# Kernel tuning notes

Hardware: AMD Instinct MI355X
Metric: run time of the kernel (lower is better)

Reference implementation:

```python
import jax, jax.numpy as jnp
import numpy as np

N_HEAD = 12


def setup_inputs() -> dict:
    key = jax.random.key(0)
    ks = jax.random.split(key, 5)
    B, T, C = 2, 2048, 768
    x = jax.random.normal(ks[0], (B, T, C), dtype=jnp.float32)
    w_attn = jax.random.normal(ks[1], (3 * C, C), dtype=jnp.float32) * 0.02
    b_attn = jax.random.normal(ks[2], (3 * C,), dtype=jnp.float32) * 0.02
    w_proj = jax.random.normal(ks[3], (C, C), dtype=jnp.float32) * 0.02
    b_proj = jax.random.normal(ks[4], (C,), dtype=jnp.float32) * 0.02
    return {"x": x, "w_attn": w_attn, "b_attn": b_attn, "w_proj": w_proj, "b_proj": b_proj}


def reference(x, w_attn, b_attn, w_proj, b_proj):
    B, T, C = x.shape
    H = N_HEAD
    D = C // H
    # fused QKV projection (torch Linear: x @ W.T + b)
    qkv = x @ w_attn.T + b_attn                      # [B, T, 3C]
    q, k, v = jnp.split(qkv, 3, axis=-1)
    q = q.reshape(B, T, H, D).transpose(0, 2, 1, 3)  # [B, H, T, D]
    k = k.reshape(B, T, H, D).transpose(0, 2, 1, 3)
    v = v.reshape(B, T, H, D).transpose(0, 2, 1, 3)
    # NOTE: original scales by 1/sqrt(k.size(0)) == 1/sqrt(B) (batch!), reproduced faithfully
    scale = 1.0 / jnp.sqrt(jnp.asarray(B, dtype=x.dtype))
    scores = jnp.einsum("bhtd,bhsd->bhts", q, k) * scale  # [B, H, T, T]
    causal = jnp.tril(jnp.ones((T, T), dtype=bool))
    scores = jnp.where(causal[None, None], scores, jnp.asarray(-jnp.inf, dtype=x.dtype))
    attn = jax.nn.softmax(scores, axis=-1)
    # dropout layers are identity in eval mode
    out = jnp.einsum("bhts,bhsd->bhtd", attn, v)     # [B, H, T, D]
    out = out.transpose(0, 2, 1, 3).reshape(B, T, C)
    return out @ w_proj.T + b_proj
```

## Files before the change

kernel.cpp:

```cpp
#include <hip/hip_runtime.h>
#include <hip/hip_bf16.h>
#include <stdint.h>

typedef __bf16 bf16;
typedef __bf16 bf16x4 __attribute__((ext_vector_type(4)));
typedef __bf16 bf16x8 __attribute__((ext_vector_type(8)));
typedef float f32x4 __attribute__((ext_vector_type(4)));

__device__ __forceinline__ f32x4 mfma16(bf16x8 a, bf16x8 b, f32x4 c) {
    return __builtin_amdgcn_mfma_f32_16x16x32_bf16(a, b, c, 0, 0, 0);
}

__device__ __forceinline__ void gload_lds16(const void* g, void* l) {
    __builtin_amdgcn_global_load_lds((__attribute__((address_space(1))) void*)g,
                                     (__attribute__((address_space(3))) void*)l,
                                     16, 0, 0);
}

__global__ void k_cast3(const float* __restrict__ x, const float* __restrict__ wa,
                        const float* __restrict__ wp, bf16* __restrict__ xb,
                        bf16* __restrict__ wab, bf16* __restrict__ wpb) {
    const int N1 = 786432, N2 = 442368, N3 = 147456;
    int i = blockIdx.x * blockDim.x + threadIdx.x;
    int stride = gridDim.x * blockDim.x;
    for (; i < N1 + N2 + N3; i += stride) {
        const float* src; bf16* dst; int j = i;
        if (j < N1)           { src = x;  dst = xb; }
        else if (j < N1 + N2) { src = wa; dst = wab; j -= N1; }
        else                  { src = wp; dst = wpb; j -= N1 + N2; }
        float4 v = reinterpret_cast<const float4*>(src)[j];
        bf16x4 o = { (bf16)v.x, (bf16)v.y, (bf16)v.z, (bf16)v.w };
        reinterpret_cast<bf16x4*>(dst)[j] = o;
    }
}

template<bool BF16_OUT>
__global__ __launch_bounds__(256) void k_gemm_bt(
        const bf16* __restrict__ A, const bf16* __restrict__ W,
        const float* __restrict__ bias, void* __restrict__ Cout,
        int M, int N, int K) {
    __shared__ bf16 As[128 * 64];
    __shared__ bf16 Ws[128 * 64];
    const int tid = threadIdx.x;
    const int l = tid & 63, w = tid >> 6;
    const int lr = l & 15, lq = l >> 4;
    const int wm = w >> 1, wn = w & 1;
    const int bm = blockIdx.y * 128, bn = blockIdx.x * 128;

    f32x4 acc[4][4] = {};

    for (int k0 = 0; k0 < K; k0 += 64) {
        __syncthreads();
        #pragma unroll
        for (int i = 0; i < 4; ++i) {
            int c = tid + i * 256;
            int row = c >> 3, j = c & 7;
            int src8 = (j ^ (row & 7)) * 8;
            gload_lds16(A + (size_t)(bm + row) * K + k0 + src8, As + c * 8);
            gload_lds16(W + (size_t)(bn + row) * K + k0 + src8, Ws + c * 8);
        }
        __syncthreads();
        bf16x8 af[2][4], wf[2][4];
        #pragma unroll
        for (int ks = 0; ks < 2; ++ks)
            #pragma unroll
            for (int f = 0; f < 4; ++f) {
                int ra = wm * 64 + f * 16 + lr;
                int rb = wn * 64 + f * 16 + lr;
                af[ks][f] = *reinterpret_cast<const bf16x8*>(
                    As + ra * 64 + (((ks * 4 + lq) ^ (lr & 7)) * 8));
                wf[ks][f] = *reinterpret_cast<const bf16x8*>(
                    Ws + rb * 64 + (((ks * 4 + lq) ^ (lr & 7)) * 8));
            }
        #pragma unroll
        for (int ks = 0; ks < 2; ++ks)
            #pragma unroll
            for (int fm = 0; fm < 4; ++fm)
                #pragma unroll
                for (int fn = 0; fn < 4; ++fn)
                    acc[fm][fn] = mfma16(af[ks][fm], wf[ks][fn], acc[fm][fn]);
    }

    #pragma unroll
    for (int fm = 0; fm < 4; ++fm) {
        #pragma unroll
        for (int fn = 0; fn < 4; ++fn) {
            int row = bm + wm * 64 + fm * 16 + lq * 4;
            int col = bn + wn * 64 + fn * 16 + lr;
            float bv = bias[col];
            #pragma unroll
            for (int r = 0; r < 4; ++r) {
                float v = acc[fm][fn][r] + bv;
                if (BF16_OUT)
                    ((bf16*)Cout)[(size_t)(row + r) * N + col] = (bf16)v;
                else
                    ((float*)Cout)[(size_t)(row + r) * N + col] = v;
            }
        }
    }
}

__global__ __launch_bounds__(256) void k_transV(const bf16* __restrict__ qkv,
                                                bf16* __restrict__ vT) {
    const int g = blockIdx.x;
    const int bh = g >> 4, tc = g & 15;
    const int h = bh % 12, b = bh / 12;
    const int t0 = tc * 128;
    __shared__ bf16 Lt[128][68];
    const bf16* src = qkv + (size_t)(b * 2048 + t0) * 2304 + 1536 + h * 64;
    const int tid = threadIdx.x;
    #pragma unroll
    for (int ii = 0; ii < 4; ++ii) {
        int tt = ii * 32 + (tid >> 3);
        int ch = tid & 7;
        bf16x8 v = *reinterpret_cast<const bf16x8*>(src + (size_t)tt * 2304 + ch * 8);
        union { bf16x8 v8; bf16x4 h4[2]; } u; u.v8 = v;
        *reinterpret_cast<bf16x4*>(&Lt[tt][ch * 8])     = u.h4[0];
        *reinterpret_cast<bf16x4*>(&Lt[tt][ch * 8 + 4]) = u.h4[1];
    }
    __syncthreads();
    bf16* dst = vT + (size_t)bh * 64 * 2048 + t0;
    const int d = tid >> 2;
    #pragma unroll
    for (int ii = 0; ii < 4; ++ii) {
        int tch = ii * 4 + (tid & 3);
        bf16x8 v;
        #pragma unroll
        for (int e = 0; e < 8; ++e) v[e] = Lt[tch * 8 + e][d];
        *reinterpret_cast<bf16x8*>(&dst[(size_t)d * 2048 + tch * 8]) = v;
    }
}

#define CLOG2E 1.02014439f

__global__ __launch_bounds__(256, 3) void k_flash_attn(
        const bf16* __restrict__ qkv, const bf16* __restrict__ vT,
        bf16* __restrict__ att, float* __restrict__ part, int mode) {
    __shared__ bf16 Ks[3][4096];
    __shared__ bf16 VTs[3][4096];

    const int tid = threadIdx.x;
    const int l = tid & 63, w = tid >> 6;
    const int lr = l & 15, lq = l >> 4;

    const int bid = blockIdx.x;
    int qb, h, b, jt0, jt1, slot;
    bool dopart;
    if (mode) {
        int bh = bid % 24, idx = bid / 24;
        h = bh % 12; b = bh / 12;
        if (idx < 16)      { qb = 16 + idx;  jt0 = 0;  jt1 = 16;     dopart = true;  slot = (bh * 16 + idx) * 2; }
        else if (idx < 32) { qb = 47 - idx;  jt0 = 16; jt1 = qb + 1; dopart = true;  slot = (bh * 16 + (qb - 16)) * 2 + 1; }
        else               { qb = 47 - idx;  jt0 = 0;  jt1 = qb + 1; dopart = false; slot = 0; }
    } else {
        const int s = bid >> 8, i = (bid >> 3) & 31, t7 = bid & 7;
        if (s == 0)      qb = i;
        else if (s == 2) qb = (i + 16) & 31;
        else             qb = (i < 8) ? (31 - 2 * i) : (i < 16) ? (30 - 2 * i)
                           : (i < 24) ? (62 - 2 * i) : (63 - 2 * i);
        const int hb = s * 8 + t7;
        h = hb % 12; b = hb / 12;
        jt0 = 0; jt1 = qb + 1; dopart = false; slot = 0;
    }

    const bf16* Qp  = qkv + (size_t)b * 2048 * 2304 + h * 64;
    const bf16* Kp  = Qp + 768;
    const bf16* Vtp = vT + (size_t)(b * 12 + h) * 64 * 2048;

    const int qr0 = qb * 64 + w * 16;

    bf16x8 qf[2];
    #pragma unroll
    for (int ks = 0; ks < 2; ++ks)
        qf[ks] = *reinterpret_cast<const bf16x8*>(
            Qp + (size_t)(qr0 + lr) * 2304 + ks * 32 + lq * 8);

    f32x4 o[4] = {};
    float lsum = 0.f;

    auto stageK = [&](int buf, int kv0) {
        #pragma unroll
        for (int ii = 0; ii < 2; ++ii) {
            int c = tid + ii * 256;
            int row = c >> 3, j = c & 7;
            gload_lds16(Kp + (size_t)(kv0 + row) * 2304 + ((j ^ (row & 7)) * 8),
                        &Ks[buf][c * 8]);
        }
    };
    auto stageV = [&](int buf, int kv0) {
        #pragma unroll
        for (int ii = 0; ii < 2; ++ii) {
            int c = tid + ii * 256;
            int row = c >> 3, j = c & 7;
            gload_lds16(Vtp + (size_t)row * 2048 + kv0 + ((j ^ (row & 7)) * 8),
                        &VTs[buf][c * 8]);
        }
    };

    stageK(0, jt0 * 64);
    stageV(0, jt0 * 64);
    const bool two = (jt1 > jt0 + 1);
    if (two) { stageK(1, jt0 * 64 + 64); stageV(1, jt0 * 64 + 64); }
    if (two) asm volatile("s_waitcnt vmcnt(4)" ::: "memory");
    else     asm volatile("s_waitcnt vmcnt(0)" ::: "memory");
    __builtin_amdgcn_s_barrier();
    asm volatile("" ::: "memory");

    for (int jt = jt0; jt < jt1; ++jt) {
        const int cur = (jt - jt0) % 3;
        const int kv0 = jt * 64;
        if (jt + 2 < jt1) {
            stageK((jt + 2 - jt0) % 3, kv0 + 128);
            stageV((jt + 2 - jt0) % 3, kv0 + 128);
        }

        const bool diag = (jt == qb);
        const int rsw = lr & 7;
        float p[4][4];
        __builtin_amdgcn_s_setprio(1);
        #pragma unroll
        for (int t = 0; t < 4; ++t) {
            f32x4 sacc = {0.f, 0.f, 0.f, 0.f};
            #pragma unroll
            for (int ks = 0; ks < 2; ++ks) {
                bf16x8 kf = *reinterpret_cast<const bf16x8*>(
                    &Ks[cur][(t * 16 + lr) * 64 + (((ks * 4 + lq) ^ rsw) * 8)]);
                sacc = mfma16(kf, qf[ks], sacc);
            }
            #pragma unroll
            for (int r = 0; r < 4; ++r)
                p[t][r] = __builtin_amdgcn_exp2f(sacc[r] * CLOG2E);
        }
        __builtin_amdgcn_s_setprio(0);
        if (diag) {
            #pragma unroll
            for (int t = 0; t < 4; ++t)
                #pragma unroll
                for (int r = 0; r < 4; ++r)
                    if (t * 16 + lq * 4 + r > w * 16 + lr) p[t][r] = 0.f;
        }
        {
            float s0 = (p[0][0] + p[0][1]) + (p[0][2] + p[0][3]);
            float s1 = (p[1][0] + p[1][1]) + (p[1][2] + p[1][3]);
            float s2 = (p[2][0] + p[2][1]) + (p[2][2] + p[2][3]);
            float s3 = (p[3][0] + p[3][1]) + (p[3][2] + p[3][3]);
            lsum += (s0 + s1) + (s2 + s3);
        }

        unsigned P0[4], P1[4];
        #pragma unroll
        for (int t = 0; t < 4; ++t) {
            asm("v_cvt_pk_bf16_f32 %0, %1, %2" : "=v"(P0[t]) : "v"(p[t][0]), "v"(p[t][1]));
            asm("v_cvt_pk_bf16_f32 %0, %1, %2" : "=v"(P1[t]) : "v"(p[t][2]), "v"(p[t][3]));
        }
        #pragma unroll
        for (int ks = 0; ks < 2; ++ks) {
            unsigned a0 = P0[2 * ks], b0 = P0[2 * ks + 1];
            asm volatile("v_permlane32_swap_b32 %0, %1" : "+v"(a0), "+v"(b0));
            asm volatile("v_permlane16_swap_b32 %0, %1" : "+v"(a0), "+v"(b0));
            unsigned a1 = P1[2 * ks], b1 = P1[2 * ks + 1];
            asm volatile("v_permlane32_swap_b32 %0, %1" : "+v"(a1), "+v"(b1));
            asm volatile("v_permlane16_swap_b32 %0, %1" : "+v"(a1), "+v"(b1));
            union { unsigned u[4]; bf16x8 v8; } pk_;
            pk_.u[0] = a0; pk_.u[1] = a1; pk_.u[2] = b0; pk_.u[3] = b1;
            bf16x8 pa = pk_.v8;
            __builtin_amdgcn_s_setprio(1);
            #pragma unroll
            for (int db = 0; db < 4; ++db) {
                bf16x8 vf = *reinterpret_cast<const bf16x8*>(
                    &VTs[cur][(db * 16 + lr) * 64 + (((ks * 4 + lq) ^ rsw) * 8)]);
                o[db] = mfma16(pa, vf, o[db]);
            }
            __builtin_amdgcn_s_setprio(0);
        }

        if (jt + 1 < jt1) {
            if (jt + 2 < jt1) asm volatile("s_waitcnt vmcnt(4)" ::: "memory");
            else              asm volatile("s_waitcnt vmcnt(0)" ::: "memory");
        }
        __builtin_amdgcn_s_barrier();
        asm volatile("" ::: "memory");
    }

    lsum += __shfl_xor(lsum, 16);
    lsum += __shfl_xor(lsum, 32);

    if (dopart) {
        float* pb = part + (size_t)slot * 4160;
        #pragma unroll
        for (int db = 0; db < 4; ++db)
            #pragma unroll
            for (int r = 0; r < 4; ++r)
                pb[(w * 16 + lq * 4 + r) * 64 + db * 16 + lr] = o[db][r];
        if (lq == 0) pb[4096 + w * 16 + lr] = lsum;
    } else {
        float inv[4];
        #pragma unroll
        for (int r = 0; r < 4; ++r)
            inv[r] = 1.0f / __shfl(lsum, lq * 4 + r);
        #pragma unroll
        for (int db = 0; db < 4; ++db)
            #pragma unroll
            for (int r = 0; r < 4; ++r) {
                float v = o[db][r] * inv[r];
                att[(size_t)(b * 2048 + qr0 + lq * 4 + r) * 768 + h * 64 + db * 16 + lr] = (bf16)v;
            }
    }
}

__global__ __launch_bounds__(256) void k_attn_reduce(
        const float* __restrict__ part, bf16* __restrict__ att) {
    int g = blockIdx.x;
    int bh = g / 16, q16 = g % 16, qb = 16 + q16;
    int h = bh % 12, b = bh / 12;
    const float* p0 = part + (size_t)((bh * 16 + q16) * 2) * 4160;
    const float* p1 = p0 + 4160;
    for (int e = threadIdx.x; e < 4096; e += 256) {
        int row = e >> 6, col = e & 63;
        float O = p0[e] + p1[e];
        float L = p0[4096 + row] + p1[4096 + row];
        att[(size_t)(b * 2048 + qb * 64 + row) * 768 + h * 64 + col] = (bf16)(O / L);
    }
}

extern "C" void kernel_launch(void* const* d_in, const int* in_sizes, int n_in,
                              void* d_out, int out_size, void* d_ws, size_t ws_size,
                              hipStream_t stream) {
    const float* x      = (const float*)d_in[0];
    const float* w_attn = (const float*)d_in[1];
    const float* b_attn = (const float*)d_in[2];
    const float* w_proj = (const float*)d_in[3];
    const float* b_proj = (const float*)d_in[4];

    char* ws = (char*)d_ws;
    bf16* xb   = (bf16*)(ws + 0);
    bf16* vT   = (bf16*)(ws + 0);
    bf16* wab  = (bf16*)(ws + 6291456);
    bf16* wpb  = (bf16*)(ws + 9830400);
    bf16* qkv  = (bf16*)(ws + 11010048);
    bf16* att  = (bf16*)(ws + 29884416);
    float* part = (float*)(ws + 36175872);
    const unsigned long long WS_NEEDED = 36175872ull + 12779520ull;

    k_cast3<<<2048, 256, 0, stream>>>(x, w_attn, w_proj, xb, wab, wpb);

    dim3 g1(2304 / 128, 4096 / 128);
    k_gemm_bt<true><<<g1, 256, 0, stream>>>(xb, wab, b_attn, qkv, 4096, 2304, 768);

    k_transV<<<384, 256, 0, stream>>>(qkv, vT);

    if (ws_size >= WS_NEEDED) {
        k_flash_attn<<<1152, 256, 0, stream>>>(qkv, vT, att, part, 1);
        k_attn_reduce<<<384, 256, 0, stream>>>(part, att);
    } else {
        k_flash_attn<<<768, 256, 0, stream>>>(qkv, vT, att, part, 0);
    }

    dim3 g2(768 / 128, 4096 / 128);
    k_gemm_bt<false><<<g2, 256, 0, stream>>>(att, wpb, b_proj, d_out, 4096, 768, 768);
}
```

Measured before the change: 91.53 us.

## Process two query tiles per attention block and narrow output-projection GEMM tile

Each flash-attention block now handles 128 query rows (two 64-row tiles) and reuses every staged K/V tile for both, halving K/V global loads and LDS staging per query row. The causal skip for the upper tile is handled with a per-iteration active flag, and the split-K partial/reduce layout is rebuilt for 128-row blocks with a new work assignment. Separately, the output-projection GEMM is templated to a 64-wide N tile, doubling its grid so more CUs are busy. The cost is more registers for doubled accumulators, fewer attention blocks in flight, and some wasted masking work on diagonal tiles.

```diff
diff --git a/kernel.cpp b/kernel.cpp
--- a/kernel.cpp
+++ b/kernel.cpp
@@ -34,20 +34,21 @@
     }
 }
 
-template<bool BF16_OUT>
+template<int BN, bool BF16_OUT>
 __global__ __launch_bounds__(256) void k_gemm_bt(
         const bf16* __restrict__ A, const bf16* __restrict__ W,
         const float* __restrict__ bias, void* __restrict__ Cout,
         int M, int N, int K) {
+    constexpr int FN = BN / 32;
     __shared__ bf16 As[128 * 64];
-    __shared__ bf16 Ws[128 * 64];
+    __shared__ bf16 Ws[BN * 64];
     const int tid = threadIdx.x;
     const int l = tid & 63, w = tid >> 6;
     const int lr = l & 15, lq = l >> 4;
     const int wm = w >> 1, wn = w & 1;
-    const int bm = blockIdx.y * 128, bn = blockIdx.x * 128;
-
-    f32x4 acc[4][4] = {};
+    const int bm = blockIdx.y * 128, bn = blockIdx.x * BN;
+
+    f32x4 acc[4][FN] = {};
 
     for (int k0 = 0; k0 < K; k0 += 64) {
         __syncthreads();
@@ -57,36 +58,46 @@
             int row = c >> 3, j = c & 7;
             int src8 = (j ^ (row & 7)) * 8;
             gload_lds16(A + (size_t)(bm + row) * K + k0 + src8, As + c * 8);
+        }
+        #pragma unroll
+        for (int i = 0; i < FN; ++i) {
+            int c = tid + i * 256;
+            int row = c >> 3, j = c & 7;
+            int src8 = (j ^ (row & 7)) * 8;
             gload_lds16(W + (size_t)(bn + row) * K + k0 + src8, Ws + c * 8);
         }
         __syncthreads();
-        bf16x8 af[2][4], wf[2][4];
-        #pragma unroll
-        for (int ks = 0; ks < 2; ++ks)
+        bf16x8 af[2][4], wf[2][FN];
+        #pragma unroll
+        for (int ks = 0; ks < 2; ++ks) {
             #pragma unroll
             for (int f = 0; f < 4; ++f) {
                 int ra = wm * 64 + f * 16 + lr;
-                int rb = wn * 64 + f * 16 + lr;
                 af[ks][f] = *reinterpret_cast<const bf16x8*>(
                     As + ra * 64 + (((ks * 4 + lq) ^ (lr & 7)) * 8));
+            }
+            #pragma unroll
+            for (int f = 0; f < FN; ++f) {
+                int rb = wn * (FN * 16) + f * 16 + lr;
                 wf[ks][f] = *reinterpret_cast<const bf16x8*>(
                     Ws + rb * 64 + (((ks * 4 + lq) ^ (lr & 7)) * 8));
             }
+        }
         #pragma unroll
         for (int ks = 0; ks < 2; ++ks)
             #pragma unroll
             for (int fm = 0; fm < 4; ++fm)
                 #pragma unroll
-                for (int fn = 0; fn < 4; ++fn)
+                for (int fn = 0; fn < FN; ++fn)
                     acc[fm][fn] = mfma16(af[ks][fm], wf[ks][fn], acc[fm][fn]);
     }
 
     #pragma unroll
     for (int fm = 0; fm < 4; ++fm) {
         #pragma unroll
-        for (int fn = 0; fn < 4; ++fn) {
+        for (int fn = 0; fn < FN; ++fn) {
             int row = bm + wm * 64 + fm * 16 + lq * 4;
-            int col = bn + wn * 64 + fn * 16 + lr;
+            int col = bn + wn * (FN * 16) + fn * 16 + lr;
             float bv = bias[col];
             #pragma unroll
             for (int r = 0; r < 4; ++r) {
@@ -147,36 +158,41 @@
     int qb, h, b, jt0, jt1, slot;
     bool dopart;
     if (mode) {
-        int bh = bid % 24, idx = bid / 24;
+        const int bh = bid / 24, idx = bid % 24;
         h = bh % 12; b = bh / 12;
-        if (idx < 16)      { qb = 16 + idx;  jt0 = 0;  jt1 = 16;     dopart = true;  slot = (bh * 16 + idx) * 2; }
-        else if (idx < 32) { qb = 47 - idx;  jt0 = 16; jt1 = qb + 1; dopart = true;  slot = (bh * 16 + (qb - 16)) * 2 + 1; }
-        else               { qb = 47 - idx;  jt0 = 0;  jt1 = qb + 1; dopart = false; slot = 0; }
+        if (idx < 16) {
+            qb = 8 + (idx >> 1);
+            const int c = idx & 1;
+            jt0 = c ? (qb + 1) : 0;
+            jt1 = c ? (2 * qb + 2) : (qb + 1);
+            dopart = true;
+            slot = (bh * 8 + (qb - 8)) * 2 + c;
+        } else {
+            qb = idx - 16;
+            jt0 = 0; jt1 = 2 * qb + 2; dopart = false; slot = 0;
+        }
     } else {
-        const int s = bid >> 8, i = (bid >> 3) & 31, t7 = bid & 7;
-        if (s == 0)      qb = i;
-        else if (s == 2) qb = (i + 16) & 31;
-        else             qb = (i < 8) ? (31 - 2 * i) : (i < 16) ? (30 - 2 * i)
-                           : (i < 24) ? (62 - 2 * i) : (63 - 2 * i);
-        const int hb = s * 8 + t7;
-        h = hb % 12; b = hb / 12;
-        jt0 = 0; jt1 = qb + 1; dopart = false; slot = 0;
+        qb = bid & 15; const int bh = bid >> 4;
+        h = bh % 12; b = bh / 12;
+        jt0 = 0; jt1 = 2 * qb + 2; dopart = false; slot = 0;
     }
 
     const bf16* Qp  = qkv + (size_t)b * 2048 * 2304 + h * 64;
     const bf16* Kp  = Qp + 768;
     const bf16* Vtp = vT + (size_t)(b * 12 + h) * 64 * 2048;
 
-    const int qr0 = qb * 64 + w * 16;
-
-    bf16x8 qf[2];
+    const int qr0 = qb * 128 + w * 16;
+
+    bf16x8 qf[2][2];
     #pragma unroll
-    for (int ks = 0; ks < 2; ++ks)
-        qf[ks] = *reinterpret_cast<const bf16x8*>(
-            Qp + (size_t)(qr0 + lr) * 2304 + ks * 32 + lq * 8);
-
-    f32x4 o[4] = {};
-    float lsum = 0.f;
+    for (int u = 0; u < 2; ++u)
+        #pragma unroll
+        for (int ks = 0; ks < 2; ++ks)
+            qf[u][ks] = *reinterpret_cast<const bf16x8*>(
+                Qp + (size_t)(qr0 + u * 64 + lr) * 2304 + ks * 32 + lq * 8);
+
+    f32x4 o[2][4] = {};
+    float lsum[2] = {0.f, 0.f};
 
     auto stageK = [&](int buf, int kv0) {
         #pragma unroll
@@ -196,57 +212,7 @@
                         &VTs[buf][c * 8]);
         }
     };
-
-    stageK(0, jt0 * 64);
-    stageV(0, jt0 * 64);
-    const bool two = (jt1 > jt0 + 1);
-    if (two) { stageK(1, jt0 * 64 + 64); stageV(1, jt0 * 64 + 64); }
-    if (two) asm volatile("s_waitcnt vmcnt(4)" ::: "memory");
-    else     asm volatile("s_waitcnt vmcnt(0)" ::: "memory");
-    __builtin_amdgcn_s_barrier();
-    asm volatile("" ::: "memory");
-
-    for (int jt = jt0; jt < jt1; ++jt) {
-        const int cur = (jt - jt0) % 3;
-        const int kv0 = jt * 64;
-        if (jt + 2 < jt1) {
-            stageK((jt + 2 - jt0) % 3, kv0 + 128);
-            stageV((jt + 2 - jt0) % 3, kv0 + 128);
-        }
-
-        const bool diag = (jt == qb);
-        const int rsw = lr & 7;
-        float p[4][4];
-        __builtin_amdgcn_s_setprio(1);
-        #pragma unroll
-        for (int t = 0; t < 4; ++t) {
-            f32x4 sacc = {0.f, 0.f, 0.f, 0.f};
-            #pragma unroll
-            for (int ks = 0; ks < 2; ++ks) {
-                bf16x8 kf = *reinterpret_cast<const bf16x8*>(
-                    &Ks[cur][(t * 16 + lr) * 64 + (((ks * 4 + lq) ^ rsw) * 8)]);
-                sacc = mfma16(kf, qf[ks], sacc);
-            }
-            #pragma unroll
-            for (int r = 0; r < 4; ++r)
-                p[t][r] = __builtin_amdgcn_exp2f(sacc[r] * CLOG2E);
-        }
-        __builtin_amdgcn_s_setprio(0);
-        if (diag) {
-            #pragma unroll
-            for (int t = 0; t < 4; ++t)
-                #pragma unroll
-                for (int r = 0; r < 4; ++r)
-                    if (t * 16 + lq * 4 + r > w * 16 + lr) p[t][r] = 0.f;
-        }
-        {
-            float s0 = (p[0][0] + p[0][1]) + (p[0][2] + p[0][3]);
-            float s1 = (p[1][0] + p[1][1]) + (p[1][2] + p[1][3]);
-            float s2 = (p[2][0] + p[2][1]) + (p[2][2] + p[2][3]);
-            float s3 = (p[3][0] + p[3][1]) + (p[3][2] + p[3][3]);
-            lsum += (s0 + s1) + (s2 + s3);
-        }
-
+    auto packP = [&](const float (&p)[4][4], bf16x8 (&pa)[2]) {
         unsigned P0[4], P1[4];
         #pragma unroll
         for (int t = 0; t < 4; ++t) {
@@ -263,16 +229,96 @@
             asm volatile("v_permlane16_swap_b32 %0, %1" : "+v"(a1), "+v"(b1));
             union { unsigned u[4]; bf16x8 v8; } pk_;
             pk_.u[0] = a0; pk_.u[1] = a1; pk_.u[2] = b0; pk_.u[3] = b1;
-            bf16x8 pa = pk_.v8;
-            __builtin_amdgcn_s_setprio(1);
+            pa[ks] = pk_.v8;
+        }
+    };
+
+    stageK(0, jt0 * 64);
+    stageV(0, jt0 * 64);
+    const bool two = (jt1 > jt0 + 1);
+    if (two) { stageK(1, jt0 * 64 + 64); stageV(1, jt0 * 64 + 64); }
+    if (two) asm volatile("s_waitcnt vmcnt(4)" ::: "memory");
+    else     asm volatile("s_waitcnt vmcnt(0)" ::: "memory");
+    __builtin_amdgcn_s_barrier();
+    asm volatile("" ::: "memory");
+
+    for (int jt = jt0; jt < jt1; ++jt) {
+        const int cur = (jt - jt0) % 3;
+        const int kv0 = jt * 64;
+        if (jt + 2 < jt1) {
+            stageK((jt + 2 - jt0) % 3, kv0 + 128);
+            stageV((jt + 2 - jt0) % 3, kv0 + 128);
+        }
+
+        const bool u0act = (jt <= 2 * qb);
+        const int rsw = lr & 7;
+        float p0[4][4], p1[4][4];
+        __builtin_amdgcn_s_setprio(1);
+        #pragma unroll
+        for (int t = 0; t < 4; ++t) {
+            bf16x8 kf0 = *reinterpret_cast<const bf16x8*>(
+                &Ks[cur][(t * 16 + lr) * 64 + ((lq ^ rsw) * 8)]);
+            bf16x8 kf1 = *reinterpret_cast<const bf16x8*>(
+                &Ks[cur][(t * 16 + lr) * 64 + (((4 + lq) ^ rsw) * 8)]);
+            f32x4 s1 = {0.f, 0.f, 0.f, 0.f};
+            s1 = mfma16(kf0, qf[1][0], s1);
+            s1 = mfma16(kf1, qf[1][1], s1);
+            #pragma unroll
+            for (int r = 0; r < 4; ++r)
+                p1[t][r] = __builtin_amdgcn_exp2f(s1[r] * CLOG2E);
+            if (u0act) {
+                f32x4 s0 = {0.f, 0.f, 0.f, 0.f};
+                s0 = mfma16(kf0, qf[0][0], s0);
+                s0 = mfma16(kf1, qf[0][1], s0);
+                #pragma unroll
+                for (int r = 0; r < 4; ++r)
+                    p0[t][r] = __builtin_amdgcn_exp2f(s0[r] * CLOG2E);
+            }
+        }
+        __builtin_amdgcn_s_setprio(0);
+        if (jt == 2 * qb) {
+            #pragma unroll
+            for (int t = 0; t < 4; ++t)
+                #pragma unroll
+                for (int r = 0; r < 4; ++r)
+                    if (t * 16 + lq * 4 + r > w * 16 + lr) p0[t][r] = 0.f;
+        }
+        if (jt == 2 * qb + 1) {
+            #pragma unroll
+            for (int t = 0; t < 4; ++t)
+                #pragma unroll
+                for (int r = 0; r < 4; ++r)
+                    if (t * 16 + lq * 4 + r > w * 16 + lr) p1[t][r] = 0.f;
+        }
+        {
+            float a = (p1[0][0] + p1[0][1]) + (p1[0][2] + p1[0][3]);
+            float c = (p1[1][0] + p1[1][1]) + (p1[1][2] + p1[1][3]);
+            float d = (p1[2][0] + p1[2][1]) + (p1[2][2] + p1[2][3]);
+            float e = (p1[3][0] + p1[3][1]) + (p1[3][2] + p1[3][3]);
+            lsum[1] += (a + c) + (d + e);
+            if (u0act) {
+                float a0 = (p0[0][0] + p0[0][1]) + (p0[0][2] + p0[0][3]);
+                float c0 = (p0[1][0] + p0[1][1]) + (p0[1][2] + p0[1][3]);
+                float d0 = (p0[2][0] + p0[2][1]) + (p0[2][2] + p0[2][3]);
+                float e0 = (p0[3][0] + p0[3][1]) + (p0[3][2] + p0[3][3]);
+                lsum[0] += (a0 + c0) + (d0 + e0);
+            }
+        }
+
+        bf16x8 pa1[2], pa0[2];
+        packP(p1, pa1);
+        if (u0act) packP(p0, pa0);
+        __builtin_amdgcn_s_setprio(1);
+        #pragma unroll
+        for (int ks = 0; ks < 2; ++ks)
             #pragma unroll
             for (int db = 0; db < 4; ++db) {
                 bf16x8 vf = *reinterpret_cast<const bf16x8*>(
                     &VTs[cur][(db * 16 + lr) * 64 + (((ks * 4 + lq) ^ rsw) * 8)]);
-                o[db] = mfma16(pa, vf, o[db]);
-            }
-            __builtin_amdgcn_s_setprio(0);
-        }
+                o[1][db] = mfma16(pa1[ks], vf, o[1][db]);
+                if (u0act) o[0][db] = mfma16(pa0[ks], vf, o[0][db]);
+            }
+        __builtin_amdgcn_s_setprio(0);
 
         if (jt + 1 < jt1) {
             if (jt + 2 < jt1) asm volatile("s_waitcnt vmcnt(4)" ::: "memory");
@@ -282,44 +328,54 @@
         asm volatile("" ::: "memory");
     }
 
-    lsum += __shfl_xor(lsum, 16);
-    lsum += __shfl_xor(lsum, 32);
+    #pragma unroll
+    for (int u = 0; u < 2; ++u) {
+        lsum[u] += __shfl_xor(lsum[u], 16);
+        lsum[u] += __shfl_xor(lsum[u], 32);
+    }
 
     if (dopart) {
-        float* pb = part + (size_t)slot * 4160;
-        #pragma unroll
-        for (int db = 0; db < 4; ++db)
+        float* pb = part + (size_t)slot * 8320;
+        #pragma unroll
+        for (int u = 0; u < 2; ++u) {
+            #pragma unroll
+            for (int db = 0; db < 4; ++db)
+                #pragma unroll
+                for (int r = 0; r < 4; ++r)
+                    pb[(u * 64 + w * 16 + lq * 4 + r) * 64 + db * 16 + lr] = o[u][db][r];
+            if (lq == 0) pb[8192 + u * 64 + w * 16 + lr] = lsum[u];
+        }
+    } else {
+        #pragma unroll
+        for (int u = 0; u < 2; ++u) {
+            float inv[4];
             #pragma unroll
             for (int r = 0; r < 4; ++r)
-                pb[(w * 16 + lq * 4 + r) * 64 + db * 16 + lr] = o[db][r];
-        if (lq == 0) pb[4096 + w * 16 + lr] = lsum;
-    } else {
-        float inv[4];
-        #pragma unroll
-        for (int r = 0; r < 4; ++r)
-            inv[r] = 1.0f / __shfl(lsum, lq * 4 + r);
-        #pragma unroll
-        for (int db = 0; db < 4; ++db)
-            #pragma unroll
-            for (int r = 0; r < 4; ++r) {
-                float v = o[db][r] * inv[r];
-                att[(size_t)(b * 2048 + qr0 + lq * 4 + r) * 768 + h * 64 + db * 16 + lr] = (bf16)v;
-            }
+                inv[r] = 1.0f / __shfl(lsum[u], lq * 4 + r);
+            #pragma unroll
+            for (int db = 0; db < 4; ++db)
+                #pragma unroll
+                for (int r = 0; r < 4; ++r) {
+                    float v = o[u][db][r] * inv[r];
+                    att[(size_t)(b * 2048 + qr0 + u * 64 + lq * 4 + r) * 768
+                        + h * 64 + db * 16 + lr] = (bf16)v;
+                }
+        }
     }
 }
 
 __global__ __launch_bounds__(256) void k_attn_reduce(
         const float* __restrict__ part, bf16* __restrict__ att) {
     int g = blockIdx.x;
-    int bh = g / 16, q16 = g % 16, qb = 16 + q16;
+    int bh = g >> 3, q8 = g & 7, qb = 8 + q8;
     int h = bh % 12, b = bh / 12;
-    const float* p0 = part + (size_t)((bh * 16 + q16) * 2) * 4160;
-    const float* p1 = p0 + 4160;
-    for (int e = threadIdx.x; e < 4096; e += 256) {
+    const float* p0 = part + (size_t)((bh * 8 + q8) * 2) * 8320;
+    const float* p1 = p0 + 8320;
+    for (int e = threadIdx.x; e < 8192; e += 256) {
         int row = e >> 6, col = e & 63;
         float O = p0[e] + p1[e];
-        float L = p0[4096 + row] + p1[4096 + row];
-        att[(size_t)(b * 2048 + qb * 64 + row) * 768 + h * 64 + col] = (bf16)(O / L);
+        float L = p0[8192 + row] + p1[8192 + row];
+        att[(size_t)(b * 2048 + qb * 128 + row) * 768 + h * 64 + col] = (bf16)(O / L);
     }
 }
 
@@ -345,17 +401,17 @@
     k_cast3<<<2048, 256, 0, stream>>>(x, w_attn, w_proj, xb, wab, wpb);
 
     dim3 g1(2304 / 128, 4096 / 128);
-    k_gemm_bt<true><<<g1, 256, 0, stream>>>(xb, wab, b_attn, qkv, 4096, 2304, 768);
+    k_gemm_bt<128, true><<<g1, 256, 0, stream>>>(xb, wab, b_attn, qkv, 4096, 2304, 768);
 
     k_transV<<<384, 256, 0, stream>>>(qkv, vT);
 
     if (ws_size >= WS_NEEDED) {
-        k_flash_attn<<<1152, 256, 0, stream>>>(qkv, vT, att, part, 1);
-        k_attn_reduce<<<384, 256, 0, stream>>>(part, att);
+        k_flash_attn<<<576, 256, 0, stream>>>(qkv, vT, att, part, 1);
+        k_attn_reduce<<<192, 256, 0, stream>>>(part, att);
     } else {
-        k_flash_attn<<<768, 256, 0, stream>>>(qkv, vT, att, part, 0);
-    }
-
-    dim3 g2(768 / 128, 4096 / 128);
-    k_gemm_bt<false><<<g2, 256, 0, stream>>>(att, wpb, b_proj, d_out, 4096, 768, 768);
-}
+        k_flash_attn<<<384, 256, 0, stream>>>(qkv, vT, att, part, 0);
+    }
+
+    dim3 g2(768 / 64, 4096 / 128);
+    k_gemm_bt<64, false><<<g2, 256, 0, stream>>>(att, wpb, b_proj, d_out, 4096, 768, 768);
+}
```

After: 102.3 us. +11.7%, slower.

## Cut attention V buffering to two stages, raise occupancy, narrow output-projection tile

Applied to the files above, without the earlier changes.

The flash-attention kernel now keeps V in a double buffer instead of a triple buffer. V is staged one tile ahead while K stays two tiles ahead, and the waitcnt thresholds are adjusted to match. This lowers LDS use so the launch bound can ask for four blocks per SM instead of three. The GEMM is templated on tile width N, and the output projection uses 64-wide N tiles, which doubles its grid from 192 blocks for better CU fill. The risks are less V prefetch slack and register pressure under the higher occupancy target.

```diff
diff --git a/kernel.cpp b/kernel.cpp
--- a/kernel.cpp
+++ b/kernel.cpp
@@ -34,20 +34,21 @@
     }
 }
 
-template<bool BF16_OUT>
+template<int BN, bool BF16_OUT>
 __global__ __launch_bounds__(256) void k_gemm_bt(
         const bf16* __restrict__ A, const bf16* __restrict__ W,
         const float* __restrict__ bias, void* __restrict__ Cout,
         int M, int N, int K) {
+    constexpr int FN = BN / 32;
     __shared__ bf16 As[128 * 64];
-    __shared__ bf16 Ws[128 * 64];
+    __shared__ bf16 Ws[BN * 64];
     const int tid = threadIdx.x;
     const int l = tid & 63, w = tid >> 6;
     const int lr = l & 15, lq = l >> 4;
     const int wm = w >> 1, wn = w & 1;
-    const int bm = blockIdx.y * 128, bn = blockIdx.x * 128;
-
-    f32x4 acc[4][4] = {};
+    const int bm = blockIdx.y * 128, bn = blockIdx.x * BN;
+
+    f32x4 acc[4][FN] = {};
 
     for (int k0 = 0; k0 < K; k0 += 64) {
         __syncthreads();
@@ -57,36 +58,46 @@
             int row = c >> 3, j = c & 7;
             int src8 = (j ^ (row & 7)) * 8;
             gload_lds16(A + (size_t)(bm + row) * K + k0 + src8, As + c * 8);
+        }
+        #pragma unroll
+        for (int i = 0; i < FN; ++i) {
+            int c = tid + i * 256;
+            int row = c >> 3, j = c & 7;
+            int src8 = (j ^ (row & 7)) * 8;
             gload_lds16(W + (size_t)(bn + row) * K + k0 + src8, Ws + c * 8);
         }
         __syncthreads();
-        bf16x8 af[2][4], wf[2][4];
-        #pragma unroll
-        for (int ks = 0; ks < 2; ++ks)
+        bf16x8 af[2][4], wf[2][FN];
+        #pragma unroll
+        for (int ks = 0; ks < 2; ++ks) {
             #pragma unroll
             for (int f = 0; f < 4; ++f) {
                 int ra = wm * 64 + f * 16 + lr;
-                int rb = wn * 64 + f * 16 + lr;
                 af[ks][f] = *reinterpret_cast<const bf16x8*>(
                     As + ra * 64 + (((ks * 4 + lq) ^ (lr & 7)) * 8));
+            }
+            #pragma unroll
+            for (int f = 0; f < FN; ++f) {
+                int rb = wn * (FN * 16) + f * 16 + lr;
                 wf[ks][f] = *reinterpret_cast<const bf16x8*>(
                     Ws + rb * 64 + (((ks * 4 + lq) ^ (lr & 7)) * 8));
             }
+        }
         #pragma unroll
         for (int ks = 0; ks < 2; ++ks)
             #pragma unroll
             for (int fm = 0; fm < 4; ++fm)
                 #pragma unroll
-                for (int fn = 0; fn < 4; ++fn)
+                for (int fn = 0; fn < FN; ++fn)
                     acc[fm][fn] = mfma16(af[ks][fm], wf[ks][fn], acc[fm][fn]);
     }
 
     #pragma unroll
     for (int fm = 0; fm < 4; ++fm) {
         #pragma unroll
-        for (int fn = 0; fn < 4; ++fn) {
+        for (int fn = 0; fn < FN; ++fn) {
             int row = bm + wm * 64 + fm * 16 + lq * 4;
-            int col = bn + wn * 64 + fn * 16 + lr;
+            int col = bn + wn * (FN * 16) + fn * 16 + lr;
             float bv = bias[col];
             #pragma unroll
             for (int r = 0; r < 4; ++r) {
@@ -133,11 +144,11 @@
 
 #define CLOG2E 1.02014439f
 
-__global__ __launch_bounds__(256, 3) void k_flash_attn(
+__global__ __launch_bounds__(256, 4) void k_flash_attn(
         const bf16* __restrict__ qkv, const bf16* __restrict__ vT,
         bf16* __restrict__ att, float* __restrict__ part, int mode) {
     __shared__ bf16 Ks[3][4096];
-    __shared__ bf16 VTs[3][4096];
+    __shared__ bf16 VTs[2][4096];
 
     const int tid = threadIdx.x;
     const int l = tid & 63, w = tid >> 6;
@@ -200,19 +211,18 @@
     stageK(0, jt0 * 64);
     stageV(0, jt0 * 64);
     const bool two = (jt1 > jt0 + 1);
-    if (two) { stageK(1, jt0 * 64 + 64); stageV(1, jt0 * 64 + 64); }
-    if (two) asm volatile("s_waitcnt vmcnt(4)" ::: "memory");
+    if (two) stageK(1, jt0 * 64 + 64);
+    if (two) asm volatile("s_waitcnt vmcnt(2)" ::: "memory");
     else     asm volatile("s_waitcnt vmcnt(0)" ::: "memory");
     __builtin_amdgcn_s_barrier();
     asm volatile("" ::: "memory");
 
     for (int jt = jt0; jt < jt1; ++jt) {
-        const int cur = (jt - jt0) % 3;
+        const int curK = (jt - jt0) % 3;
+        const int curV = (jt - jt0) & 1;
         const int kv0 = jt * 64;
-        if (jt + 2 < jt1) {
-            stageK((jt + 2 - jt0) % 3, kv0 + 128);
-            stageV((jt + 2 - jt0) % 3, kv0 + 128);
-        }
+        if (jt + 1 < jt1) stageV(curV ^ 1, kv0 + 64);
+        if (jt + 2 < jt1) stageK((jt + 2 - jt0) % 3, kv0 + 128);
 
         const bool diag = (jt == qb);
         const int rsw = lr & 7;
@@ -224,7 +234,7 @@
             #pragma unroll
             for (int ks = 0; ks < 2; ++ks) {
                 bf16x8 kf = *reinterpret_cast<const bf16x8*>(
-                    &Ks[cur][(t * 16 + lr) * 64 + (((ks * 4 + lq) ^ rsw) * 8)]);
+                    &Ks[curK][(t * 16 + lr) * 64 + (((ks * 4 + lq) ^ rsw) * 8)]);
                 sacc = mfma16(kf, qf[ks], sacc);
             }
             #pragma unroll
@@ -268,14 +278,14 @@
             #pragma unroll
             for (int db = 0; db < 4; ++db) {
                 bf16x8 vf = *reinterpret_cast<const bf16x8*>(
-                    &VTs[cur][(db * 16 + lr) * 64 + (((ks * 4 + lq) ^ rsw) * 8)]);
+                    &VTs[curV][(db * 16 + lr) * 64 + (((ks * 4 + lq) ^ rsw) * 8)]);
                 o[db] = mfma16(pa, vf, o[db]);
             }
             __builtin_amdgcn_s_setprio(0);
         }
 
         if (jt + 1 < jt1) {
-            if (jt + 2 < jt1) asm volatile("s_waitcnt vmcnt(4)" ::: "memory");
+            if (jt + 2 < jt1) asm volatile("s_waitcnt vmcnt(2)" ::: "memory");
             else              asm volatile("s_waitcnt vmcnt(0)" ::: "memory");
         }
         __builtin_amdgcn_s_barrier();
@@ -345,7 +355,7 @@
     k_cast3<<<2048, 256, 0, stream>>>(x, w_attn, w_proj, xb, wab, wpb);
 
     dim3 g1(2304 / 128, 4096 / 128);
-    k_gemm_bt<true><<<g1, 256, 0, stream>>>(xb, wab, b_attn, qkv, 4096, 2304, 768);
+    k_gemm_bt<128, true><<<g1, 256, 0, stream>>>(xb, wab, b_attn, qkv, 4096, 2304, 768);
 
     k_transV<<<384, 256, 0, stream>>>(qkv, vT);
 
@@ -356,6 +366,6 @@
         k_flash_attn<<<768, 256, 0, stream>>>(qkv, vT, att, part, 0);
     }
 
-    dim3 g2(768 / 128, 4096 / 128);
-    k_gemm_bt<false><<<g2, 256, 0, stream>>>(att, wpb, b_proj, d_out, 4096, 768, 768);
-}
+    dim3 g2(768 / 64, 4096 / 128);
+    k_gemm_bt<64, false><<<g2, 256, 0, stream>>>(att, wpb, b_proj, d_out, 4096, 768, 768);
+}
```

Result: faster. 89.26 us (-2.5%).
